# Kernel optimization log

Measured on AMD Instinct MI355X. Metric: run time of the kernel, lower is better.

## Reference

```python
import jax, jax.numpy as jnp
import numpy as np

WS = 7      # window size
SHIFT = 3   # shift size
H = 56
W = 56
NH = 16     # num heads


def _layernorm(x, g, b):
    m = x.mean(-1, keepdims=True)
    v = x.var(-1, keepdims=True)
    return (x - m) / jnp.sqrt(v + 1e-5) * g + b


def setup_inputs() -> dict:
    key = jax.random.key(0)
    ks = jax.random.split(key, 8)
    B, C = 16, 512
    DH = 4 * C
    s = 0.02
    x = jax.random.normal(ks[0], (B, H * W, C), jnp.float32)

    # relative position index (matches torch buffer construction)
    coords = np.stack(np.meshgrid(np.arange(WS), np.arange(WS), indexing='ij')).reshape(2, -1)
    rel = (coords[:, :, None] - coords[:, None, :]).transpose(1, 2, 0).copy()
    rel[..., 0] += WS - 1
    rel[..., 1] += WS - 1
    rel[..., 0] *= 2 * WS - 1
    rpi = jnp.asarray(rel.sum(-1), jnp.int32)  # (49, 49)

    # shifted-window additive attention mask (nW, N, N)
    img = np.zeros((H, W))
    cnt = 0
    for hs in (slice(0, -WS), slice(-WS, -SHIFT), slice(-SHIFT, None)):
        for wsl in (slice(0, -WS), slice(-WS, -SHIFT), slice(-SHIFT, None)):
            img[hs, wsl] = cnt
            cnt += 1
    mw = img.reshape(H // WS, WS, W // WS, WS).transpose(0, 2, 1, 3).reshape(-1, WS * WS)
    diff = mw[:, None, :] - mw[:, :, None]  # == mw.unsqueeze(1) - mw.unsqueeze(2)
    attn_mask = jnp.asarray(np.where(diff != 0, -100.0, 0.0), jnp.float32)

    return {
        'x': x,
        'rpi': rpi,
        'attn_mask': attn_mask,
        'norm1_g': jnp.ones((C,), jnp.float32),
        'norm1_b': jnp.zeros((C,), jnp.float32),
        'qkv_w': jax.random.normal(ks[1], (3 * C, C), jnp.float32) * s,
        'qkv_b': jnp.zeros((3 * C,), jnp.float32),
        'proj_w': jax.random.normal(ks[2], (C, C), jnp.float32) * s,
        'proj_b': jnp.zeros((C,), jnp.float32),
        'rpb_table': jax.random.normal(ks[3], ((2 * WS - 1) ** 2, NH), jnp.float32) * s,
        'norm2_g': jnp.ones((C,), jnp.float32),
        'norm2_b': jnp.zeros((C,), jnp.float32),
        'mlp_w1': jax.random.normal(ks[4], (DH, C), jnp.float32) * s,
        'mlp_b1': jnp.zeros((DH,), jnp.float32),
        'mlp_w2': jax.random.normal(ks[5], (C, DH), jnp.float32) * s,
        'mlp_b2': jnp.zeros((C,), jnp.float32),
    }


def reference(x, rpi, attn_mask, norm1_g, norm1_b, qkv_w, qkv_b, proj_w, proj_b,
              rpb_table, norm2_g, norm2_b, mlp_w1, mlp_b1, mlp_w2, mlp_b2):
    B, L, C = x.shape
    N = WS * WS
    nW = (H // WS) * (W // WS)
    hd = C // NH

    # --- attention branch ---
    h = _layernorm(x, norm1_g, norm1_b).reshape(B, H, W, C)
    h = jnp.roll(h, (-SHIFT, -SHIFT), axis=(1, 2))
    # window partition -> (B*nW, N, C)
    xw = h.reshape(B, H // WS, WS, W // WS, WS, C).transpose(0, 1, 3, 2, 4, 5).reshape(B * nW, N, C)

    qkv = (xw @ qkv_w.T + qkv_b).reshape(B * nW, N, 3, NH, hd).transpose(2, 0, 3, 1, 4)
    q, k, v = qkv[0], qkv[1], qkv[2]  # (B*nW, NH, N, hd)
    attn = jnp.einsum('bhnd,bhmd->bhnm', q * (hd ** -0.5), k)
    rpb = rpb_table[rpi].transpose(2, 0, 1)  # (NH, N, N)
    attn = attn + rpb[None]
    attn = attn.reshape(B, nW, NH, N, N) + attn_mask[None, :, None]
    attn = jax.nn.softmax(attn.reshape(B * nW, NH, N, N), axis=-1)
    o = jnp.einsum('bhnm,bhmd->bhnd', attn, v).transpose(0, 2, 1, 3).reshape(B * nW, N, C)
    o = o @ proj_w.T + proj_b
    # window reverse + unshift
    o = o.reshape(B, H // WS, W // WS, WS, WS, C).transpose(0, 1, 3, 2, 4, 5).reshape(B, H, W, C)
    o = jnp.roll(o, (SHIFT, SHIFT), axis=(1, 2)).reshape(B, L, C)

    x = x + o
    # --- MLP branch ---
    h2 = _layernorm(x, norm2_g, norm2_b)
    m = jax.nn.gelu(h2 @ mlp_w1.T + mlp_b1, approximate=False)
    return x + (m @ mlp_w2.T + mlp_b2)
```

## Files before the change

### kernel.cpp

```cpp
#include <hip/hip_runtime.h>
#include <hip/hip_bf16.h>

typedef __attribute__((ext_vector_type(8))) short bf16x8_t;
typedef __attribute__((ext_vector_type(4))) float f32x4_t;

__device__ __forceinline__ void gll16(const void* g, void* l) {
  __builtin_amdgcn_global_load_lds((const __attribute__((address_space(1))) void*)g,
                                   (__attribute__((address_space(3))) void*)l, 16, 0, 0);
}

__global__ __launch_bounds__(256) void k_cvt(const float* __restrict__ in,
                                             __hip_bfloat16* __restrict__ out, int n) {
  int i = blockIdx.x * 256 + threadIdx.x;
  if (i < n) out[i] = __float2bfloat16(in[i]);
}

__global__ __launch_bounds__(256) void k_cmb(const int* __restrict__ rpi,
                                             const float* __restrict__ tab,
                                             const float* __restrict__ mask,
                                             float* __restrict__ cmbp) {
  int idx = blockIdx.x * 256 + threadIdx.x;
  int jj = idx & 3, lane = (idx >> 2) & 63, tile = (idx >> 8) & 15;
  int h = (idx >> 12) & 15, w6 = idx >> 16;
  int r = (tile >> 2) * 16 + (lane >> 4) * 4 + jj;
  int c = (tile & 3) * 16 + (lane & 15);
  float v = -1e9f;
  if (r < 49 && c < 49) v = tab[rpi[r * 49 + c] * 16 + h] + mask[w6 * 2401 + r * 49 + c];
  cmbp[idx] = v;
}

template<int PERM>
__global__ __launch_bounds__(256) void k_ln(const float* __restrict__ in,
                                            const float* __restrict__ g,
                                            const float* __restrict__ bta,
                                            __hip_bfloat16* __restrict__ out) {
  int token = blockIdx.x;
  int t = threadIdx.x;
  const float2 v = ((const float2*)(in + (size_t)token * 512))[t];
  float s = v.x + v.y, sq = v.x * v.x + v.y * v.y;
  #pragma unroll
  for (int d = 1; d < 64; d <<= 1) { s += __shfl_xor(s, d); sq += __shfl_xor(sq, d); }
  __shared__ float ps[4], pq[4];
  int w = t >> 6;
  if ((t & 63) == 0) { ps[w] = s; pq[w] = sq; }
  __syncthreads();
  s  = ps[0] + ps[1] + ps[2] + ps[3];
  sq = pq[0] + pq[1] + pq[2] + pq[3];
  float mean = s * (1.f / 512.f);
  float inv = rsqrtf(sq * (1.f / 512.f) - mean * mean + 1e-5f);
  size_t dst;
  if (PERM) {
    int b = token / 3136, p = token - b * 3136;
    int i = p / 56, j = p - i * 56;
    int gi = (i + 53) % 56, gj = (j + 53) % 56;
    dst = ((size_t)(((b * 64) + (gi / 7) * 8 + (gj / 7)) * 49) + (gi % 7) * 7 + (gj % 7)) * 512;
  } else {
    dst = (size_t)token * 512;
  }
  int c = t * 2;
  out[dst + c]     = __float2bfloat16((v.x - mean) * inv * g[c] + bta[c]);
  out[dst + c + 1] = __float2bfloat16((v.y - mean) * inv * g[c + 1] + bta[c + 1]);
}

__global__ __launch_bounds__(256) void k_attn(const __hip_bfloat16* __restrict__ qkv,
                                              const float* __restrict__ cmbp,
                                              __hip_bfloat16* __restrict__ o) {
  __shared__ __align__(16) __hip_bfloat16 vt_all[4 * 32 * 72];
  __shared__ __align__(16) __hip_bfloat16 P_all[4 * 64 * 72];
  const int t = threadIdx.x, l = t & 63, w = t >> 6;
  const int bw = blockIdx.x;
  const int head = blockIdx.y * 4 + w;
  const int rr = l & 15, g = l >> 4;
  __hip_bfloat16* vt = vt_all + w * (32 * 72);
  __hip_bfloat16* P  = P_all  + w * (64 * 72);
  const __hip_bfloat16* base = qkv + (size_t)bw * 49 * 1536 + head * 32;
  const bf16x8_t zero8 = {};

  { int d = l >> 1, sg = (l & 1) * 8;
    *(bf16x8_t*)(vt + d * 72 + 48 + sg) = zero8; }
  __builtin_amdgcn_sched_barrier(0);
  #pragma unroll
  for (int it = 0; it < 4; ++it) {
    int idx = l + it * 64;
    if (idx < 196) {
      int j = idx >> 2, sg = (idx & 3) * 8;
      bf16x8_t vv = *(const bf16x8_t*)(base + 1024 + (size_t)j * 1536 + sg);
      #pragma unroll
      for (int s2 = 0; s2 < 8; ++s2) vt[(sg + s2) * 72 + j] = ((__hip_bfloat16*)&vv)[s2];
    }
  }
  bf16x8_t aq[4], bk[4];
  #pragma unroll
  for (int m = 0; m < 4; ++m) {
    int row = m * 16 + rr;
    aq[m] = (row < 49) ? *(const bf16x8_t*)(base + (size_t)row * 1536 + g * 8) : zero8;
    bk[m] = (row < 49) ? *(const bf16x8_t*)(base + 512 + (size_t)row * 1536 + g * 8) : zero8;
  }
  const float4* cp = (const float4*)(cmbp + (size_t)((bw & 63) * 16 + head) * 4096);
  f32x4_t S[4][4];
  #pragma unroll
  for (int tm = 0; tm < 4; ++tm)
    #pragma unroll
    for (int tn = 0; tn < 4; ++tn) {
      float4 cv = cp[(tm * 4 + tn) * 64 + l];
      f32x4_t c0 = { cv.x, cv.y, cv.z, cv.w };
      S[tm][tn] = __builtin_amdgcn_mfma_f32_16x16x32_bf16(aq[tm], bk[tn], c0, 0, 0, 0);
    }
  float sm[4][4];
  #pragma unroll
  for (int tm = 0; tm < 4; ++tm) {
    #pragma unroll
    for (int jj = 0; jj < 4; ++jj) {
      float v = fmaxf(fmaxf(S[tm][0][jj], S[tm][1][jj]), fmaxf(S[tm][2][jj], S[tm][3][jj]));
      v = fmaxf(v, __shfl_xor(v, 1));
      v = fmaxf(v, __shfl_xor(v, 2));
      v = fmaxf(v, __shfl_xor(v, 4));
      v = fmaxf(v, __shfl_xor(v, 8));
      float s = 0.f;
      #pragma unroll
      for (int tn = 0; tn < 4; ++tn) {
        float e = __expf(S[tm][tn][jj] - v);
        S[tm][tn][jj] = e;
        s += e;
      }
      s += __shfl_xor(s, 1); s += __shfl_xor(s, 2); s += __shfl_xor(s, 4); s += __shfl_xor(s, 8);
      sm[tm][jj] = s;
    }
  }
  #pragma unroll
  for (int tm = 0; tm < 4; ++tm)
    #pragma unroll
    for (int tn = 0; tn < 4; ++tn)
      #pragma unroll
      for (int jj = 0; jj < 4; ++jj)
        P[(tm * 16 + g * 4 + jj) * 72 + tn * 16 + rr] = __float2bfloat16(S[tm][tn][jj]);

  f32x4_t O[4][2] = {};
  #pragma unroll
  for (int ks = 0; ks < 2; ++ks) {
    bf16x8_t pa[4], vb[2];
    #pragma unroll
    for (int tm = 0; tm < 4; ++tm)
      pa[tm] = *(const bf16x8_t*)(P + (tm * 16 + rr) * 72 + ks * 32 + g * 8);
    #pragma unroll
    for (int tn = 0; tn < 2; ++tn)
      vb[tn] = *(const bf16x8_t*)(vt + (tn * 16 + rr) * 72 + ks * 32 + g * 8);
    #pragma unroll
    for (int tm = 0; tm < 4; ++tm)
      #pragma unroll
      for (int tn = 0; tn < 2; ++tn)
        O[tm][tn] = __builtin_amdgcn_mfma_f32_16x16x32_bf16(pa[tm], vb[tn], O[tm][tn], 0, 0, 0);
  }
  #pragma unroll
  for (int tm = 0; tm < 4; ++tm) {
    #pragma unroll
    for (int jj = 0; jj < 4; ++jj) {
      int r = tm * 16 + g * 4 + jj;
      if (r < 49) {
        float rcp = 1.f / sm[tm][jj];
        size_t ob = ((size_t)bw * 49 + r) * 512 + head * 32;
        o[ob + rr]      = __float2bfloat16(O[tm][0][jj] * rcp);
        o[ob + 16 + rr] = __float2bfloat16(O[tm][1][jj] * rcp);
      }
    }
  }
}

template<int EP>
__global__ __launch_bounds__(512, 2) void gemm256(const __hip_bfloat16* __restrict__ A,
                                                  const __hip_bfloat16* __restrict__ Bw,
                                                  int K, int Ncols, int nNB,
                                                  const float* __restrict__ bias,
                                                  __hip_bfloat16* __restrict__ obf,
                                                  const float* __restrict__ resid,
                                                  float* __restrict__ ofp) {
  __shared__ __align__(16) char LDS[131072];
  const int nwg = gridDim.x, orig = blockIdx.x;
  const int q8 = nwg >> 3, r8 = nwg & 7;
  const int xcd = orig & 7, lin = orig >> 3;
  const int wgid = (xcd < r8 ? xcd * (q8 + 1) : r8 * (q8 + 1) + (xcd - r8) * q8) + lin;
  const int bx = wgid / nNB, by = wgid - bx * nNB;
  const int m0 = bx * 256, n0 = by * 256;
  const int t = threadIdx.x, l = t & 63, w = t >> 6;
  const int wr = w >> 2, wc = w & 3;
  const int rr = l & 15, kq = l >> 4;
  const int lofs = rr * 64 + ((kq * 16) ^ ((rr & 8) << 2));

  size_t o0, o1;
  { int d = t * 16; int r = (d >> 10) * 16 + ((d >> 6) & 15);
    int cb = (d & 63) ^ (((d >> 9) & 1) << 5); o0 = (size_t)r * K + (cb >> 1); }
  { int d = 8192 + t * 16; int r = (d >> 10) * 16 + ((d >> 6) & 15);
    int cb = (d & 63) ^ (((d >> 9) & 1) << 5); o1 = (size_t)r * K + (cb >> 1); }
  const __hip_bfloat16* gA = A + (size_t)m0 * K;
  const __hip_bfloat16* gB = Bw + (size_t)n0 * K;

  auto stage = [&](int tile, int half) {
    int b = (tile & 3) * 16384 + half * 8192 + t * 16;
    size_t o = (half ? o1 : o0) + (size_t)tile * 32;
    gll16(gA + o, LDS + b);
    gll16(gB + o, LDS + 65536 + b);
  };

  f32x4_t acc[8][4] = {};

  stage(0, 0); stage(0, 1); stage(1, 0); stage(1, 1); stage(2, 0); stage(2, 1);
  asm volatile("s_waitcnt vmcnt(8)" ::: "memory");
  __builtin_amdgcn_s_barrier();

  const int NT = K >> 5;
  for (int kt = 0; kt < NT; ++kt) {
    const char* bA = LDS + (kt & 3) * 16384 + wr * 8192;
    const char* bB = LDS + 65536 + (kt & 3) * 16384 + wc * 4096;
    bf16x8_t ar[4], br[4];
    #pragma unroll
    for (int m = 0; m < 4; ++m) ar[m] = *(const bf16x8_t*)(bA + m * 1024 + lofs);
    #pragma unroll
    for (int n = 0; n < 4; ++n) br[n] = *(const bf16x8_t*)(bB + n * 1024 + lofs);
    if (kt + 3 < NT) stage(kt + 3, 0);
    __builtin_amdgcn_s_barrier();
    asm volatile("s_waitcnt lgkmcnt(0)" ::: "memory");
    __builtin_amdgcn_sched_barrier(0);
    __builtin_amdgcn_s_setprio(1);
    #pragma unroll
    for (int m = 0; m < 4; ++m)
      #pragma unroll
      for (int n = 0; n < 4; ++n)
        acc[m][n] = __builtin_amdgcn_mfma_f32_16x16x32_bf16(ar[m], br[n], acc[m][n], 0, 0, 0);
    __builtin_amdgcn_s_setprio(0);
    __builtin_amdgcn_s_barrier();
    #pragma unroll
    for (int m = 0; m < 4; ++m) ar[m] = *(const bf16x8_t*)(bA + (4 + m) * 1024 + lofs);
    if (kt + 3 < NT) stage(kt + 3, 1);
    __builtin_amdgcn_s_barrier();
    asm volatile("s_waitcnt lgkmcnt(0)" ::: "memory");
    __builtin_amdgcn_sched_barrier(0);
    __builtin_amdgcn_s_setprio(1);
    #pragma unroll
    for (int m = 0; m < 4; ++m)
      #pragma unroll
      for (int n = 0; n < 4; ++n)
        acc[4 + m][n] = __builtin_amdgcn_mfma_f32_16x16x32_bf16(ar[m], br[n], acc[4 + m][n], 0, 0, 0);
    __builtin_amdgcn_s_setprio(0);
    if (kt + 3 < NT)      asm volatile("s_waitcnt vmcnt(8)" ::: "memory");
    else if (kt + 2 < NT) asm volatile("s_waitcnt vmcnt(4)" ::: "memory");
    else if (kt + 1 < NT) asm volatile("s_waitcnt vmcnt(0)" ::: "memory");
    __builtin_amdgcn_s_barrier();
  }

  #pragma unroll
  for (int m = 0; m < 8; ++m) {
    #pragma unroll
    for (int n = 0; n < 4; ++n) {
      const int gcol = n0 + wc * 64 + n * 16 + rr;
      #pragma unroll
      for (int j = 0; j < 4; ++j) {
        const int grow = m0 + wr * 128 + m * 16 + kq * 4 + j;
        float v = acc[m][n][j] + bias[gcol];
        if (EP == 0) {
          if (gcol < 512) v *= 0.17677669529663687f;
          obf[(size_t)grow * Ncols + gcol] = __float2bfloat16(v);
        } else if (EP == 1) {
          int bw = grow / 49, nn = grow - bw * 49;
          int b = bw >> 6, wi = bw & 63;
          int hh = (wi >> 3) * 7 + nn / 7 + 3;  if (hh >= 56) hh -= 56;
          int ww2 = (wi & 7) * 7 + (nn % 7) + 3; if (ww2 >= 56) ww2 -= 56;
          size_t tok = (size_t)b * 3136 + hh * 56 + ww2;
          ofp[tok * 512 + gcol] = resid[tok * 512 + gcol] + v;
        } else if (EP == 2) {
          float u = 0.5f * v * (1.f + erff(v * 0.70710678118f));
          obf[(size_t)grow * Ncols + gcol] = __float2bfloat16(u);
        } else {
          ofp[(size_t)grow * 512 + gcol] += v;
        }
      }
    }
  }
}

extern "C" void kernel_launch(void* const* d_in, const int* in_sizes, int n_in,
                              void* d_out, int out_size, void* d_ws, size_t ws_size,
                              hipStream_t stream) {
  const float* x      = (const float*)d_in[0];
  const int*   rpi    = (const int*)  d_in[1];
  const float* amask  = (const float*)d_in[2];
  const float* n1g    = (const float*)d_in[3];
  const float* n1b    = (const float*)d_in[4];
  const float* qkv_w  = (const float*)d_in[5];
  const float* qkv_b  = (const float*)d_in[6];
  const float* proj_w = (const float*)d_in[7];
  const float* proj_b = (const float*)d_in[8];
  const float* rpb_t  = (const float*)d_in[9];
  const float* n2g    = (const float*)d_in[10];
  const float* n2b    = (const float*)d_in[11];
  const float* w1     = (const float*)d_in[12];
  const float* b1     = (const float*)d_in[13];
  const float* w2     = (const float*)d_in[14];
  const float* b2     = (const float*)d_in[15];
  float* out = (float*)d_out;

  char* ws = (char*)d_ws;
  const size_t M = 50176;
  const size_t szA = M * 2048 * 2;
  const size_t szB = M * 1536 * 2;
  const size_t offB = szA;
  const size_t offW = offB + szB;
  __hip_bfloat16* bufA = (__hip_bfloat16*)(ws);
  __hip_bfloat16* bufB = (__hip_bfloat16*)(ws + offB);
  __hip_bfloat16* wqkv  = (__hip_bfloat16*)(ws + offW);
  __hip_bfloat16* wproj = wqkv + 786432;
  __hip_bfloat16* wm1   = wproj + 262144;
  __hip_bfloat16* wm2   = wm1 + 1048576;
  float* cmbp = (float*)(ws + szA - (size_t)4194304 * 4);

  k_cvt<<<3072, 256, 0, stream>>>(qkv_w, wqkv, 786432);
  k_cvt<<<1024, 256, 0, stream>>>(proj_w, wproj, 262144);
  k_cvt<<<4096, 256, 0, stream>>>(w1, wm1, 1048576);
  k_cvt<<<4096, 256, 0, stream>>>(w2, wm2, 1048576);
  k_cmb<<<16384, 256, 0, stream>>>(rpi, rpb_t, amask, cmbp);

  k_ln<1><<<50176, 256, 0, stream>>>(x, n1g, n1b, bufA);
  gemm256<0><<<196 * 6, 512, 0, stream>>>(bufA, wqkv, 512, 1536, 6, qkv_b, bufB, nullptr, nullptr);
  k_attn<<<dim3(1024, 4), 256, 0, stream>>>(bufB, cmbp, bufA);
  gemm256<1><<<196 * 2, 512, 0, stream>>>(bufA, wproj, 512, 512, 2, proj_b, nullptr, x, out);
  k_ln<0><<<50176, 256, 0, stream>>>(out, n2g, n2b, bufB);
  gemm256<2><<<196 * 8, 512, 0, stream>>>(bufB, wm1, 512, 2048, 8, b1, bufA, nullptr, nullptr);
  gemm256<3><<<196 * 2, 512, 0, stream>>>(bufA, wm2, 2048, 512, 2, b2, nullptr, nullptr, out);
}
```

Baseline: 843.2 us.

## Replace direct global-to-LDS loads with register-staged prefetch in GEMM

Swaps the global_load_lds DMA path for ordinary 16-byte global loads into registers, which are written to swizzled LDS one tile later. Prefetch runs one tile ahead in registers with three LDS buffers in flight, and the explicit vmcnt waits are removed. The aim is to use ordinary load-and-store scheduling, which may pipeline better, at the cost of extra VGPRs and explicit LDS write instructions. The correctness of the LDS writes now depends on compiler-inserted waits on the register loads.

Result: slower. 922.5 us (+9.4%).

```diff
diff --git a/kernel.cpp b/kernel.cpp
--- a/kernel.cpp
+++ b/kernel.cpp
@@ -4,10 +4,7 @@
 typedef __attribute__((ext_vector_type(8))) short bf16x8_t;
 typedef __attribute__((ext_vector_type(4))) float f32x4_t;
 
-__device__ __forceinline__ void gll16(const void* g, void* l) {
-  __builtin_amdgcn_global_load_lds((const __attribute__((address_space(1))) void*)g,
-                                   (__attribute__((address_space(3))) void*)l, 16, 0, 0);
-}
+#define LD8(p) (*(const bf16x8_t*)(p))
 
 __global__ __launch_bounds__(256) void k_cvt(const float* __restrict__ in,
                                              __hip_bfloat16* __restrict__ out, int n) {
@@ -186,28 +183,42 @@
   const int rr = l & 15, kq = l >> 4;
   const int lofs = rr * 64 + ((kq * 16) ^ ((rr & 8) << 2));
 
-  size_t o0, o1;
-  { int d = t * 16; int r = (d >> 10) * 16 + ((d >> 6) & 15);
-    int cb = (d & 63) ^ (((d >> 9) & 1) << 5); o0 = (size_t)r * K + (cb >> 1); }
-  { int d = 8192 + t * 16; int r = (d >> 10) * 16 + ((d >> 6) & 15);
-    int cb = (d & 63) ^ (((d >> 9) & 1) << 5); o1 = (size_t)r * K + (cb >> 1); }
-  const __hip_bfloat16* gA = A + (size_t)m0 * K;
-  const __hip_bfloat16* gB = Bw + (size_t)n0 * K;
-
-  auto stage = [&](int tile, int half) {
-    int b = (tile & 3) * 16384 + half * 8192 + t * 16;
-    size_t o = (half ? o1 : o0) + (size_t)tile * 32;
-    gll16(gA + o, LDS + b);
-    gll16(gB + o, LDS + 65536 + b);
+  int rs0, cs0, rs1, cs1;
+  { int d = t * 16;        rs0 = (d >> 10) * 16 + ((d >> 6) & 15); cs0 = (d & 63) >> 1; }
+  { int d = 8192 + t * 16; rs1 = (d >> 10) * 16 + ((d >> 6) & 15); cs1 = (d & 63) >> 1; }
+  const __hip_bfloat16* gA0 = A  + (size_t)(m0 + rs0) * K + cs0;
+  const __hip_bfloat16* gA1 = A  + (size_t)(m0 + rs1) * K + cs1;
+  const __hip_bfloat16* gB0 = Bw + (size_t)(n0 + rs0) * K + cs0;
+  const __hip_bfloat16* gB1 = Bw + (size_t)(n0 + rs1) * K + cs1;
+  const int d0i = t * 16, d1i = 8192 + t * 16;
+  const int wz0 = (d0i & ~63) | ((d0i & 63) ^ (((d0i >> 9) & 1) << 5));
+  const int wz1 = (d1i & ~63) | ((d1i & 63) ^ (((d1i >> 9) & 1) << 5));
+
+  bf16x8_t sa0, sa1, sb0, sb1;
+  auto loadS = [&](int tile) {
+    int c = tile * 32;
+    sa0 = LD8(gA0 + c); sa1 = LD8(gA1 + c);
+    sb0 = LD8(gB0 + c); sb1 = LD8(gB1 + c);
   };
+  auto writeSA = [&](int tile) {
+    char* d = LDS + (tile & 3) * 16384;
+    *(bf16x8_t*)(d + wz0) = sa0; *(bf16x8_t*)(d + wz1) = sa1;
+  };
+  auto writeSB = [&](int tile) {
+    char* d = LDS + 65536 + (tile & 3) * 16384;
+    *(bf16x8_t*)(d + wz0) = sb0; *(bf16x8_t*)(d + wz1) = sb1;
+  };
 
   f32x4_t acc[8][4] = {};
 
-  stage(0, 0); stage(0, 1); stage(1, 0); stage(1, 1); stage(2, 0); stage(2, 1);
-  asm volatile("s_waitcnt vmcnt(8)" ::: "memory");
+  const int NT = K >> 5;
+  loadS(0); writeSA(0); writeSB(0);
+  loadS(1); writeSA(1); writeSB(1);
+  loadS(2); writeSA(2); writeSB(2);
+  loadS(3);
+  asm volatile("s_waitcnt lgkmcnt(0)" ::: "memory");
   __builtin_amdgcn_s_barrier();
 
-  const int NT = K >> 5;
   for (int kt = 0; kt < NT; ++kt) {
     const char* bA = LDS + (kt & 3) * 16384 + wr * 8192;
     const char* bB = LDS + 65536 + (kt & 3) * 16384 + wc * 4096;
@@ -216,7 +227,7 @@
     for (int m = 0; m < 4; ++m) ar[m] = *(const bf16x8_t*)(bA + m * 1024 + lofs);
     #pragma unroll
     for (int n = 0; n < 4; ++n) br[n] = *(const bf16x8_t*)(bB + n * 1024 + lofs);
-    if (kt + 3 < NT) stage(kt + 3, 0);
+    if (kt + 3 < NT) writeSA(kt + 3);
     __builtin_amdgcn_s_barrier();
     asm volatile("s_waitcnt lgkmcnt(0)" ::: "memory");
     __builtin_amdgcn_sched_barrier(0);
@@ -230,7 +241,8 @@
     __builtin_amdgcn_s_barrier();
     #pragma unroll
     for (int m = 0; m < 4; ++m) ar[m] = *(const bf16x8_t*)(bA + (4 + m) * 1024 + lofs);
-    if (kt + 3 < NT) stage(kt + 3, 1);
+    if (kt + 3 < NT) writeSB(kt + 3);
+    if (kt + 4 < NT) loadS(kt + 4);
     __builtin_amdgcn_s_barrier();
     asm volatile("s_waitcnt lgkmcnt(0)" ::: "memory");
     __builtin_amdgcn_sched_barrier(0);
@@ -241,9 +253,6 @@
       for (int n = 0; n < 4; ++n)
         acc[4 + m][n] = __builtin_amdgcn_mfma_f32_16x16x32_bf16(ar[m], br[n], acc[4 + m][n], 0, 0, 0);
     __builtin_amdgcn_s_setprio(0);
-    if (kt + 3 < NT)      asm volatile("s_waitcnt vmcnt(8)" ::: "memory");
-    else if (kt + 2 < NT) asm volatile("s_waitcnt vmcnt(4)" ::: "memory");
-    else if (kt + 1 < NT) asm volatile("s_waitcnt vmcnt(0)" ::: "memory");
     __builtin_amdgcn_s_barrier();
   }
 
```

## Restructure GEMM main loop to K=64 double-buffered tiles with quadrant staging

Applied to the files above, without the earlier changes.

Reworks the 256x256 bf16 GEMM mainloop. Each iteration now covers a 64-wide K tile held in two LDS buffers instead of 32-wide tiles in a four-deep ring. Global-to-LDS staging is split into A and B halves and interleaved between four MFMA quadrant phases, which halves the number of loop iterations and barriers per K. The intent is better overlap of loads with matrix ops and fewer synchronisations. The risks are higher register pressure from holding more fragments and shallower prefetch depth, so memory latency may be exposed.

Measured after the change: 808.0 us. 4.2% less time.

```diff
diff --git a/kernel.cpp b/kernel.cpp
--- a/kernel.cpp
+++ b/kernel.cpp
@@ -3,6 +3,8 @@
 
 typedef __attribute__((ext_vector_type(8))) short bf16x8_t;
 typedef __attribute__((ext_vector_type(4))) float f32x4_t;
+
+#define LD8(p) (*(const bf16x8_t*)(p))
 
 __device__ __forceinline__ void gll16(const void* g, void* l) {
   __builtin_amdgcn_global_load_lds((const __attribute__((address_space(1))) void*)g,
@@ -184,66 +186,93 @@
   const int t = threadIdx.x, l = t & 63, w = t >> 6;
   const int wr = w >> 2, wc = w & 3;
   const int rr = l & 15, kq = l >> 4;
-  const int lofs = rr * 64 + ((kq * 16) ^ ((rr & 8) << 2));
-
-  size_t o0, o1;
-  { int d = t * 16; int r = (d >> 10) * 16 + ((d >> 6) & 15);
-    int cb = (d & 63) ^ (((d >> 9) & 1) << 5); o0 = (size_t)r * K + (cb >> 1); }
-  { int d = 8192 + t * 16; int r = (d >> 10) * 16 + ((d >> 6) & 15);
-    int cb = (d & 63) ^ (((d >> 9) & 1) << 5); o1 = (size_t)r * K + (cb >> 1); }
+  const int swzo = (kq * 16) ^ ((rr & 8) << 2);
+
+  int rs0, cs0, rs1, cs1;
+  { int d = t * 16;  rs0 = (d >> 10) * 16 + ((d >> 6) & 15);
+    cs0 = ((d & 63) ^ (((d >> 9) & 1) << 5)) >> 1; }
+  { int d = 8192 + t * 16; int dd = d & 8191;
+    rs1 = (dd >> 10) * 16 + ((dd >> 6) & 15);
+    cs1 = 32 + (((d & 63) ^ (((d >> 9) & 1) << 5)) >> 1); }
   const __hip_bfloat16* gA = A + (size_t)m0 * K;
   const __hip_bfloat16* gB = Bw + (size_t)n0 * K;
 
-  auto stage = [&](int tile, int half) {
-    int b = (tile & 3) * 16384 + half * 8192 + t * 16;
-    size_t o = (half ? o1 : o0) + (size_t)tile * 32;
-    gll16(gA + o, LDS + b);
-    gll16(gB + o, LDS + 65536 + b);
+  auto stageA = [&](int T, int h) {
+    char* dst = LDS + (T & 1) * 32768 + h * 16384 + t * 16;
+    const size_t kb = (size_t)T * 64;
+    gll16(gA + (size_t)(h * 128 + rs0) * K + kb + cs0, dst);
+    gll16(gA + (size_t)(h * 128 + rs1) * K + kb + cs1, dst + 8192);
+  };
+  auto stageB = [&](int T, int h) {
+    char* dst = LDS + 65536 + (T & 1) * 32768 + h * 16384 + t * 16;
+    const size_t kb = (size_t)T * 64;
+    gll16(gB + (size_t)(h * 128 + rs0) * K + kb + cs0, dst);
+    gll16(gB + (size_t)(h * 128 + rs1) * K + kb + cs1, dst + 8192);
+  };
+
+  auto ldA = [&](bf16x8_t (&a)[4][2], int buf, int mq) {
+    const char* b = LDS + buf * 32768 + wr * 16384;
+    #pragma unroll
+    for (int m = 0; m < 4; ++m)
+      #pragma unroll
+      for (int ks = 0; ks < 2; ++ks)
+        a[m][ks] = *(const bf16x8_t*)(b + ks * 8192 + (mq * 4 + m) * 1024 + rr * 64 + swzo);
+  };
+  auto ldB = [&](bf16x8_t (&bv)[2][2], int buf, int nq) {
+    const char* b = LDS + 65536 + buf * 32768 + (wc >> 1) * 16384;
+    #pragma unroll
+    for (int n = 0; n < 2; ++n)
+      #pragma unroll
+      for (int ks = 0; ks < 2; ++ks)
+        bv[n][ks] = *(const bf16x8_t*)(b + ks * 8192 + ((wc & 1) * 4 + nq * 2 + n) * 1024 + rr * 64 + swzo);
   };
 
   f32x4_t acc[8][4] = {};
-
-  stage(0, 0); stage(0, 1); stage(1, 0); stage(1, 1); stage(2, 0); stage(2, 1);
-  asm volatile("s_waitcnt vmcnt(8)" ::: "memory");
+  auto mma = [&](bf16x8_t (&a)[4][2], bf16x8_t (&bv)[2][2], int mq, int nq) {
+    __builtin_amdgcn_s_setprio(1);
+    #pragma unroll
+    for (int m = 0; m < 4; ++m)
+      #pragma unroll
+      for (int n = 0; n < 2; ++n)
+        #pragma unroll
+        for (int ks = 0; ks < 2; ++ks)
+          acc[mq * 4 + m][nq * 2 + n] =
+            __builtin_amdgcn_mfma_f32_16x16x32_bf16(a[m][ks], bv[n][ks], acc[mq * 4 + m][nq * 2 + n], 0, 0, 0);
+    __builtin_amdgcn_s_setprio(0);
+  };
+
+  const int NT = K >> 6;
+  stageA(0, 0); stageB(0, 0); stageA(0, 1); stageB(0, 1);
+  if (1 < NT) { stageA(1, 0); stageB(1, 0); }
+  if (1 < NT) asm volatile("s_waitcnt vmcnt(4)" ::: "memory");
+  else        asm volatile("s_waitcnt vmcnt(0)" ::: "memory");
   __builtin_amdgcn_s_barrier();
 
-  const int NT = K >> 5;
   for (int kt = 0; kt < NT; ++kt) {
-    const char* bA = LDS + (kt & 3) * 16384 + wr * 8192;
-    const char* bB = LDS + 65536 + (kt & 3) * 16384 + wc * 4096;
-    bf16x8_t ar[4], br[4];
-    #pragma unroll
-    for (int m = 0; m < 4; ++m) ar[m] = *(const bf16x8_t*)(bA + m * 1024 + lofs);
-    #pragma unroll
-    for (int n = 0; n < 4; ++n) br[n] = *(const bf16x8_t*)(bB + n * 1024 + lofs);
-    if (kt + 3 < NT) stage(kt + 3, 0);
-    __builtin_amdgcn_s_barrier();
+    const int cur = kt & 1;
+    bf16x8_t Alo[4][2], Ahi[4][2], B0[2][2], B1[2][2];
+    ldA(Alo, cur, 0); ldB(B0, cur, 0);
+    if (kt + 1 < NT) stageA(kt + 1, 1);
     asm volatile("s_waitcnt lgkmcnt(0)" ::: "memory");
     __builtin_amdgcn_sched_barrier(0);
-    __builtin_amdgcn_s_setprio(1);
-    #pragma unroll
-    for (int m = 0; m < 4; ++m)
-      #pragma unroll
-      for (int n = 0; n < 4; ++n)
-        acc[m][n] = __builtin_amdgcn_mfma_f32_16x16x32_bf16(ar[m], br[n], acc[m][n], 0, 0, 0);
-    __builtin_amdgcn_s_setprio(0);
-    __builtin_amdgcn_s_barrier();
-    #pragma unroll
-    for (int m = 0; m < 4; ++m) ar[m] = *(const bf16x8_t*)(bA + (4 + m) * 1024 + lofs);
-    if (kt + 3 < NT) stage(kt + 3, 1);
-    __builtin_amdgcn_s_barrier();
+    mma(Alo, B0, 0, 0);
+    ldA(Ahi, cur, 1);
+    if (kt + 1 < NT) stageB(kt + 1, 1);
     asm volatile("s_waitcnt lgkmcnt(0)" ::: "memory");
     __builtin_amdgcn_sched_barrier(0);
-    __builtin_amdgcn_s_setprio(1);
-    #pragma unroll
-    for (int m = 0; m < 4; ++m)
-      #pragma unroll
-      for (int n = 0; n < 4; ++n)
-        acc[4 + m][n] = __builtin_amdgcn_mfma_f32_16x16x32_bf16(ar[m], br[n], acc[4 + m][n], 0, 0, 0);
-    __builtin_amdgcn_s_setprio(0);
-    if (kt + 3 < NT)      asm volatile("s_waitcnt vmcnt(8)" ::: "memory");
-    else if (kt + 2 < NT) asm volatile("s_waitcnt vmcnt(4)" ::: "memory");
-    else if (kt + 1 < NT) asm volatile("s_waitcnt vmcnt(0)" ::: "memory");
+    mma(Ahi, B0, 1, 0);
+    __builtin_amdgcn_s_barrier();
+    ldB(B1, cur, 1);
+    if (kt + 2 < NT) stageA(kt + 2, 0);
+    asm volatile("s_waitcnt lgkmcnt(0)" ::: "memory");
+    __builtin_amdgcn_sched_barrier(0);
+    mma(Ahi, B1, 1, 1);
+    if (kt + 2 < NT) stageB(kt + 2, 0);
+    mma(Alo, B1, 0, 1);
+    if (kt + 1 < NT) {
+      if (kt + 2 < NT) asm volatile("s_waitcnt vmcnt(4)" ::: "memory");
+      else             asm volatile("s_waitcnt vmcnt(0)" ::: "memory");
+    }
     __builtin_amdgcn_s_barrier();
   }
 
```

## Restructure GEMM main loop to K=64 double-buffered tiles with 4-phase MFMA schedule

Applied to the files above, without the earlier changes.

Reworks the 256x256 bf16 GEMM mainloop to stage K=64 tiles into two LDS buffers per operand instead of four K=32 buffers. It uses a new row-major XOR-swizzled LDS layout (128-byte rows, 8-way chunk swizzle) and splits each tile into four quadrant phases. Each phase interleaves LDS fragment reads, async global-to-LDS loads for the other operand or buffer, and a block of 16 MFMAs. The aim is to cut barriers per K step and overlap loads with compute more finely. The cost is more live fragment registers, and K must be a multiple of 128.

Result: faster. 825.9 us (-2.1%).

```diff
diff --git a/kernel.cpp b/kernel.cpp
--- a/kernel.cpp
+++ b/kernel.cpp
@@ -184,68 +184,94 @@
   const int t = threadIdx.x, l = t & 63, w = t >> 6;
   const int wr = w >> 2, wc = w & 3;
   const int rr = l & 15, kq = l >> 4;
-  const int lofs = rr * 64 + ((kq * 16) ^ ((rr & 8) << 2));
-
-  size_t o0, o1;
-  { int d = t * 16; int r = (d >> 10) * 16 + ((d >> 6) & 15);
-    int cb = (d & 63) ^ (((d >> 9) & 1) << 5); o0 = (size_t)r * K + (cb >> 1); }
-  { int d = 8192 + t * 16; int r = (d >> 10) * 16 + ((d >> 6) & 15);
-    int cb = (d & 63) ^ (((d >> 9) & 1) << 5); o1 = (size_t)r * K + (cb >> 1); }
+  const int gx = rr & 7;
+
+  const int srow = t >> 3;
+  const int scol = (((t & 7) ^ ((t >> 3) & 7)) << 3);
   const __hip_bfloat16* gA = A + (size_t)m0 * K;
   const __hip_bfloat16* gB = Bw + (size_t)n0 * K;
 
-  auto stage = [&](int tile, int half) {
-    int b = (tile & 3) * 16384 + half * 8192 + t * 16;
-    size_t o = (half ? o1 : o0) + (size_t)tile * 32;
-    gll16(gA + o, LDS + b);
-    gll16(gB + o, LDS + 65536 + b);
+  auto stage = [&](int arr, int buf, int rh, int T) {
+    char* dst = LDS + arr * 65536 + buf * 32768 + rh * 16384 + t * 16;
+    const __hip_bfloat16* g = (arr ? gB : gA) + (size_t)(rh * 128 + srow) * K + T * 64 + scol;
+    gll16(g, dst);
+    gll16(g + (size_t)64 * K, dst + 8192);
   };
+  auto rdA = [&](bf16x8_t (&a)[4][2], int buf, int mq) {
+    const char* b = LDS + buf * 32768 + wr * 16384;
+    #pragma unroll
+    for (int m = 0; m < 4; ++m) {
+      int r = mq * 64 + m * 16 + rr;
+      #pragma unroll
+      for (int ks = 0; ks < 2; ++ks)
+        a[m][ks] = *(const bf16x8_t*)(b + r * 128 + ((((ks << 2) + kq) ^ gx) << 4));
+    }
+  };
+  auto rdB = [&](bf16x8_t (&bv)[2][2], int buf, int nq) {
+    const char* b = LDS + 65536 + buf * 32768 + (wc >> 1) * 16384;
+    #pragma unroll
+    for (int n = 0; n < 2; ++n) {
+      int r = (wc & 1) * 64 + (nq * 2 + n) * 16 + rr;
+      #pragma unroll
+      for (int ks = 0; ks < 2; ++ks)
+        bv[n][ks] = *(const bf16x8_t*)(b + r * 128 + ((((ks << 2) + kq) ^ gx) << 4));
+    }
+  };
 
   f32x4_t acc[8][4] = {};
-
-  stage(0, 0); stage(0, 1); stage(1, 0); stage(1, 1); stage(2, 0); stage(2, 1);
-  asm volatile("s_waitcnt vmcnt(8)" ::: "memory");
+  auto mma = [&](bf16x8_t (&a)[4][2], bf16x8_t (&bv)[2][2], int mq, int nq) {
+    #pragma unroll
+    for (int m = 0; m < 4; ++m)
+      #pragma unroll
+      for (int n = 0; n < 2; ++n)
+        #pragma unroll
+        for (int ks = 0; ks < 2; ++ks)
+          acc[mq * 4 + m][nq * 2 + n] =
+            __builtin_amdgcn_mfma_f32_16x16x32_bf16(a[m][ks], bv[n][ks], acc[mq * 4 + m][nq * 2 + n], 0, 0, 0);
+  };
+
+#define PH_SYNC  __builtin_amdgcn_s_barrier();                          \
+                 asm volatile("s_waitcnt lgkmcnt(0)" ::: "memory");     \
+                 __builtin_amdgcn_sched_barrier(0);                     \
+                 __builtin_amdgcn_s_setprio(1)
+#define PH_END   __builtin_amdgcn_s_setprio(0); __builtin_amdgcn_s_barrier()
+
+  const int NT = K >> 6, ITERS = NT >> 1;
+  stage(0, 0, 0, 0); stage(0, 0, 1, 0); stage(1, 0, 0, 0); stage(1, 0, 1, 0);
+  stage(0, 1, 0, 1); stage(0, 1, 1, 1);
+  asm volatile("s_waitcnt vmcnt(4)" ::: "memory");
   __builtin_amdgcn_s_barrier();
 
-  const int NT = K >> 5;
-  for (int kt = 0; kt < NT; ++kt) {
-    const char* bA = LDS + (kt & 3) * 16384 + wr * 8192;
-    const char* bB = LDS + 65536 + (kt & 3) * 16384 + wc * 4096;
-    bf16x8_t ar[4], br[4];
-    #pragma unroll
-    for (int m = 0; m < 4; ++m) ar[m] = *(const bf16x8_t*)(bA + m * 1024 + lofs);
-    #pragma unroll
-    for (int n = 0; n < 4; ++n) br[n] = *(const bf16x8_t*)(bB + n * 1024 + lofs);
-    if (kt + 3 < NT) stage(kt + 3, 0);
+  bf16x8_t Am0[4][2], Am1[4][2], Bn0[2][2], Bn1[2][2];
+  for (int it = 0; it < ITERS; ++it) {
+    const int tE = 2 * it;
+    const bool nl = (it + 1 < ITERS);
+    rdA(Am0, 0, 0); rdB(Bn0, 0, 0); stage(1, 1, 0, tE + 1);
+    PH_SYNC; mma(Am0, Bn0, 0, 0); PH_END;
+    rdA(Am1, 0, 1); stage(1, 1, 1, tE + 1);
+    PH_SYNC; mma(Am1, Bn0, 1, 0); PH_END;
+    rdB(Bn1, 0, 1); if (nl) stage(0, 0, 0, tE + 2);
+    PH_SYNC; mma(Am1, Bn1, 1, 1); PH_END;
+    if (nl) stage(0, 0, 1, tE + 2);
+    PH_SYNC; mma(Am0, Bn1, 0, 1);
+    __builtin_amdgcn_s_setprio(0);
+    if (nl) asm volatile("s_waitcnt vmcnt(4)" ::: "memory");
+    else    asm volatile("s_waitcnt vmcnt(0)" ::: "memory");
     __builtin_amdgcn_s_barrier();
-    asm volatile("s_waitcnt lgkmcnt(0)" ::: "memory");
-    __builtin_amdgcn_sched_barrier(0);
-    __builtin_amdgcn_s_setprio(1);
-    #pragma unroll
-    for (int m = 0; m < 4; ++m)
-      #pragma unroll
-      for (int n = 0; n < 4; ++n)
-        acc[m][n] = __builtin_amdgcn_mfma_f32_16x16x32_bf16(ar[m], br[n], acc[m][n], 0, 0, 0);
+    rdA(Am0, 1, 0); rdB(Bn0, 1, 0); if (nl) stage(1, 0, 0, tE + 2);
+    PH_SYNC; mma(Am0, Bn0, 0, 0); PH_END;
+    rdA(Am1, 1, 1); if (nl) stage(1, 0, 1, tE + 2);
+    PH_SYNC; mma(Am1, Bn0, 1, 0); PH_END;
+    rdB(Bn1, 1, 1); if (nl) stage(0, 1, 0, tE + 3);
+    PH_SYNC; mma(Am1, Bn1, 1, 1); PH_END;
+    if (nl) stage(0, 1, 1, tE + 3);
+    PH_SYNC; mma(Am0, Bn1, 0, 1);
     __builtin_amdgcn_s_setprio(0);
+    if (nl) asm volatile("s_waitcnt vmcnt(4)" ::: "memory");
     __builtin_amdgcn_s_barrier();
-    #pragma unroll
-    for (int m = 0; m < 4; ++m) ar[m] = *(const bf16x8_t*)(bA + (4 + m) * 1024 + lofs);
-    if (kt + 3 < NT) stage(kt + 3, 1);
-    __builtin_amdgcn_s_barrier();
-    asm volatile("s_waitcnt lgkmcnt(0)" ::: "memory");
-    __builtin_amdgcn_sched_barrier(0);
-    __builtin_amdgcn_s_setprio(1);
-    #pragma unroll
-    for (int m = 0; m < 4; ++m)
-      #pragma unroll
-      for (int n = 0; n < 4; ++n)
-        acc[4 + m][n] = __builtin_amdgcn_mfma_f32_16x16x32_bf16(ar[m], br[n], acc[4 + m][n], 0, 0, 0);
-    __builtin_amdgcn_s_setprio(0);
-    if (kt + 3 < NT)      asm volatile("s_waitcnt vmcnt(8)" ::: "memory");
-    else if (kt + 2 < NT) asm volatile("s_waitcnt vmcnt(4)" ::: "memory");
-    else if (kt + 1 < NT) asm volatile("s_waitcnt vmcnt(0)" ::: "memory");
-    __builtin_amdgcn_s_barrier();
-  }
+  }
+#undef PH_SYNC
+#undef PH_END
 
   #pragma unroll
   for (int m = 0; m < 8; ++m) {
```
